# Kernel tuning notes

Measured on AMD Instinct MI355X. Metric: run time of the kernel, lower is better.

## Reference

```python
import jax, jax.numpy as jnp
import numpy as np
from jax import lax

DISP = 4   # max displacement for correlation -> 81 channels
KSZ = 3    # deform/gate conv kernel size


def conv2d(x, w, b=None):
    out = lax.conv_general_dilated(x, w, (1, 1), 'SAME',
                                   dimension_numbers=('NCHW', 'OIHW', 'NCHW'))
    if b is not None:
        out = out + b[None, :, None, None]
    return out


def correlation(x1, x2, d=DISP):
    # FlowNet-style cost volume, kernel_size=1: per-displacement channel-mean dot product.
    B, C, H, W = x1.shape
    x2p = jnp.pad(x2, ((0, 0), (0, 0), (d, d), (d, d)))
    outs = []
    for dy in range(2 * d + 1):
        for dx in range(2 * d + 1):
            shifted = lax.dynamic_slice(x2p, (0, 0, dy, dx), (B, C, H, W))
            outs.append(jnp.sum(x1 * shifted, axis=1) / C)
    return jnp.stack(outs, axis=1)  # [B, (2d+1)^2, H, W]


def bilinear_sample(img, y, x):
    # img: [B,C,H,W]; y,x: [B,H,W] float sample coords; zero padding outside.
    B, C, H, W = img.shape
    y0 = jnp.floor(y); x0 = jnp.floor(x)
    y1 = y0 + 1.0;     x1 = x0 + 1.0
    wy1 = y - y0; wx1 = x - x0
    wy0 = 1.0 - wy1; wx0 = 1.0 - wx1
    flat = img.reshape(B, C, H * W)

    def gather(yi, xi):
        valid = (yi >= 0) & (yi <= H - 1) & (xi >= 0) & (xi <= W - 1)
        yc = jnp.clip(yi, 0, H - 1).astype(jnp.int32)
        xc = jnp.clip(xi, 0, W - 1).astype(jnp.int32)
        idx = (yc * W + xc).reshape(B, 1, H * W)
        g = jnp.take_along_axis(flat, idx, axis=2).reshape(B, C, H, W)
        return g * valid.astype(img.dtype)[:, None]

    return (gather(y0, x0) * (wy0 * wx0)[:, None]
          + gather(y0, x1) * (wy0 * wx1)[:, None]
          + gather(y1, x0) * (wy1 * wx0)[:, None]
          + gather(y1, x1) * (wy1 * wx1)[:, None])


def deform_conv(img, offset, w, k=KSZ):
    # offset: [B, 2*k*k, H, W] with (dy, dx) pairs per kernel tap (row-major).
    B, C, H, W = img.shape
    pad = (k - 1) // 2
    ys = jnp.arange(H, dtype=img.dtype)[None, :, None]
    xs = jnp.arange(W, dtype=img.dtype)[None, None, :]
    out = jnp.zeros((B, w.shape[0], H, W), dtype=img.dtype)
    for kk in range(k * k):
        ky, kx = kk // k, kk % k
        y = ys + (ky - pad) + offset[:, 2 * kk]
        x = xs + (kx - pad) + offset[:, 2 * kk + 1]
        s = bilinear_sample(img, y, x)
        out = out + jnp.einsum('oc,bchw->bohw', w[:, :, ky, kx], s)
    return out


def linear_scale(x, std_multiplier=3.0):
    pos = x > 0
    cnt = jnp.sum(pos).astype(x.dtype)
    mean = jnp.sum(jnp.where(pos, x, 0.0)) / jnp.maximum(cnt, 1.0)
    var = jnp.sum(jnp.where(pos, (x - mean) ** 2, 0.0)) / jnp.maximum(cnt - 1.0, 1.0)
    ub = mean + std_multiplier * jnp.sqrt(var)
    ub = jnp.where(cnt >= 2.0, ub, 1.0)  # matches torch nan / empty-positive fallback
    return jnp.clip(x, 0.0, lax.stop_gradient(ub)) / ub


def setup_inputs() -> dict:
    key = jax.random.key(0)
    ks = jax.random.split(key, 10)
    B, C, H, W = 8, 256, 64, 64
    f = jnp.float32
    inp = {
        'inputs':   jax.random.normal(ks[0], (B, C, H, W), f),
        'in_state': jax.random.normal(ks[1], (B, C, H, W), f),
        'w_reset':  jax.random.normal(ks[2], (C, 2 * C, 3, 3), f) * 0.02,
        'b_reset':  jnp.zeros((C,), f),
        'w_update': jax.random.normal(ks[3], (C, 2 * C, 3, 3), f) * 0.02,
        'b_update': jnp.zeros((C,), f),
        'w_out':    jax.random.normal(ks[4], (C, 2 * C, 3, 3), f) * 0.02,
        'b_out':    jnp.zeros((C,), f),
        'w_offset': jax.random.normal(ks[5], (18, 81, 1, 1), f) * 0.01,
        'w_align':  jax.random.normal(ks[6], (C, C, 3, 3), f) * 0.01,
    }
    return inp


def reference(inputs, in_state, w_reset, b_reset, w_update, b_update,
              w_out, b_out, w_offset, w_align):
    # align_features: correlation -> 1x1 offset conv -> deformable conv
    corr = correlation(inputs, in_state)
    offset = conv2d(corr, w_offset)
    aligned = deform_conv(in_state, offset, w_align)
    # ConvGRU gates with linear-scaled relu gates
    stacked = jnp.concatenate([inputs, aligned], axis=1)
    update = linear_scale(jax.nn.relu(conv2d(stacked, w_update, b_update)))
    reset = linear_scale(jax.nn.relu(conv2d(stacked, w_reset, b_reset)))
    out_in = jax.nn.relu(conv2d(jnp.concatenate([inputs, in_state * reset], axis=1), w_out, b_out))
    new_state = in_state * (1.0 - update) + out_in * update
    return (new_state, new_state)  # (out_feat, new_state)
```

## Files before the change

kernel.cpp:

```cpp
#include <hip/hip_runtime.h>
#include <stdint.h>
#include <math.h>

typedef unsigned short u16;
typedef short bf16x8 __attribute__((ext_vector_type(8)));
typedef float f32x4 __attribute__((ext_vector_type(4)));

#define MFMA16x16x32(a,b,c) __builtin_amdgcn_mfma_f32_16x16x32_bf16((a),(b),(c),0,0,0)

typedef __attribute__((address_space(3))) void as3_void;
typedef const __attribute__((address_space(1))) void as1_void;

__device__ __forceinline__ void g2l16(const void* g, void* l){
#if __has_builtin(__builtin_amdgcn_global_load_lds)
  __builtin_amdgcn_global_load_lds((as1_void*)g, (as3_void*)l, 16, 0, 0);
#else
  *(int4*)l = *(const int4*)g;
#endif
}

__device__ __forceinline__ u16 f2bf(float f){
  uint32_t u = __builtin_bit_cast(uint32_t, f);
  u += 0x7fffu + ((u >> 16) & 1u);
  return (u16)(u >> 16);
}
__device__ __forceinline__ float bf2f(u16 h){
  uint32_t u = ((uint32_t)h) << 16;
  return __builtin_bit_cast(float, u);
}
__device__ __forceinline__ void unpack8(int4 v, float* o){
  uint32_t w0=(uint32_t)v.x, w1=(uint32_t)v.y, w2=(uint32_t)v.z, w3=(uint32_t)v.w;
  o[0]=__builtin_bit_cast(float, w0<<16); o[1]=__builtin_bit_cast(float, w0&0xffff0000u);
  o[2]=__builtin_bit_cast(float, w1<<16); o[3]=__builtin_bit_cast(float, w1&0xffff0000u);
  o[4]=__builtin_bit_cast(float, w2<<16); o[5]=__builtin_bit_cast(float, w2&0xffff0000u);
  o[6]=__builtin_bit_cast(float, w3<<16); o[7]=__builtin_bit_cast(float, w3&0xffff0000u);
}
__device__ __forceinline__ int iclampi(int v,int lo,int hi){ return v<lo?lo:(v>hi?hi:v); }

__global__ void k_repack(const float* __restrict__ w_reset, const float* __restrict__ b_reset,
                         const float* __restrict__ w_update, const float* __restrict__ b_update,
                         const float* __restrict__ w_out, const float* __restrict__ w_offset,
                         const float* __restrict__ w_align,
                         u16* __restrict__ wgate, u16* __restrict__ wout,
                         u16* __restrict__ walign, float* __restrict__ woff,
                         float* __restrict__ biascat){
  int idx = blockIdx.x * 256 + threadIdx.x;
  if (idx < 512*4608){
    int e = idx & 7, j = (idx >> 3) & 2047, chunk = idx >> 14;
    int nb = chunk & 1, kk = chunk >> 1;
    int l = j & 15, q = (j >> 4) & 3, t16 = (j >> 6) & 15, ks2 = j >> 10;
    int n = nb*256 + t16*16 + l;
    int tap = kk >> 3, ksin = kk & 7;
    int c = ksin*64 + ks2*32 + q*8 + e;
    int ky = tap/3, kx = tap%3;
    float v = (n < 256) ? w_update[((n*512 + c)*3 + ky)*3 + kx]
                        : w_reset[(((n-256)*512 + c)*3 + ky)*3 + kx];
    wgate[idx] = f2bf(v);
  }
  if (idx < 256*4608){
    int e = idx & 7, j = (idx >> 3) & 1023, chunk = idx >> 13;
    int nb = chunk & 1, kk = chunk >> 1;
    int l = j & 15, q = (j >> 4) & 3, t8 = (j >> 6) & 7, ks2 = j >> 9;
    int n = nb*128 + t8*16 + l;
    int tap = kk >> 3, ksin = kk & 7;
    int c = ksin*64 + ks2*32 + q*8 + e;
    int ky = tap/3, kx = tap%3;
    wout[idx] = f2bf(w_out[((n*512 + c)*3 + ky)*3 + kx]);
  }
  if (idx < 256*2304){
    int n = idx / 2304, k = idx % 2304;
    int tap = k >> 8, c = k & 255;
    int ky = tap/3, kx = tap%3;
    walign[idx] = f2bf(w_align[((n*256 + c)*3 + ky)*3 + kx]);
  }
  if (idx < 1458) woff[idx] = w_offset[idx] * (1.f/256.f);
  if (idx < 512) biascat[idx] = (idx < 256) ? b_update[idx] : b_reset[idx-256];
}

__global__ __launch_bounds__(256) void k_transform(const float* __restrict__ inputs,
    const float* __restrict__ in_state, u16* __restrict__ stacked,
    u16* __restrict__ stacked2, u16* __restrict__ x2pad){
  __shared__ u16 t1[64*264];
  __shared__ u16 t2[64*264];
  int tid = threadIdx.x, bh = blockIdx.x;
  int b = bh >> 6, h = bh & 63;
  int w = tid & 63, cq = tid >> 6;
  for (int i = 0; i < 64; ++i){
    int c = i*4 + cq;
    int gi = ((b*256 + c)*64 + h)*64 + w;
    t1[w*264 + c] = f2bf(inputs[gi]);
    t2[w*264 + c] = f2bf(in_state[gi]);
  }
  __syncthreads();
  int px = tid >> 2, cg = tid & 3;
#pragma unroll
  for (int u = 0; u < 8; ++u){
    int c = cg*64 + u*8;
    int4 v1 = *(const int4*)(t1 + px*264 + c);
    int4 v2 = *(const int4*)(t2 + px*264 + c);
    *(int4*)(stacked  + (((b*66 + h+1)*66) + (px+1))*512 + c) = v1;
    *(int4*)(stacked2 + (((b*66 + h+1)*66) + (px+1))*512 + c) = v1;
    *(int4*)(x2pad    + (((b*72 + h+4)*72) + (px+4))*256 + c) = v2;
  }
}

__global__ __launch_bounds__(256) void k_corr(const u16* __restrict__ stacked,
    const u16* __restrict__ x2pad, float* __restrict__ corr){
  __shared__ u16 lA[8192];
  __shared__ u16 lB[32768];
  int tid = threadIdx.x, idx = blockIdx.x;
  int b = idx >> 6, ty = (idx >> 3) & 7, tx = idx & 7;
  int h0 = ty*8, w0 = tx*8;
  int wave = tid >> 6, lane = tid & 63, l15 = lane & 15, quad = lane >> 4;
  f32x4 acc[4][4];
#pragma unroll
  for (int i=0;i<4;i++)
#pragma unroll
    for (int j=0;j<4;j++){ f32x4 z = {0.f,0.f,0.f,0.f}; acc[i][j] = z; }

  for (int s = 0; s < 2; ++s){
#pragma unroll
    for (int i = 0; i < 4; ++i){
      int j = tid + i*256;
      int ml = j & 15, q = (j>>4)&3, mt = (j>>6)&3, ks = j >> 8;
      int px = mt*16 + ml, py = px >> 3, pxx = px & 7;
      const u16* g = stacked + (((b*66 + h0+py+1)*66) + (w0+pxx+1))*512 + s*128 + ks*32 + q*8;
      g2l16(g, lA + j*8);
    }
#pragma unroll
    for (int i = 0; i < 16; ++i){
      int j = tid + i*256;
      int nl = j & 15, q = (j>>4)&3, nt = (j>>6)&15, ks = j >> 10;
      int qp = nt*16 + nl, qy = qp >> 4, qx = qp & 15;
      const u16* g = x2pad + (((b*72 + h0+qy)*72) + (w0+qx))*256 + s*128 + ks*32 + q*8;
      g2l16(g, lB + j*8);
    }
    __syncthreads();
#pragma unroll
    for (int ks = 0; ks < 4; ++ks){
      bf16x8 bv[4];
#pragma unroll
      for (int ni=0; ni<4; ++ni){
        int nt = wave*4 + ni;
        bv[ni] = *(const bf16x8*)(lB + (((ks*16 + nt)*4 + quad)*16 + l15)*8);
      }
#pragma unroll
      for (int mi=0; mi<4; ++mi){
        bf16x8 av = *(const bf16x8*)(lA + (((ks*4 + mi)*4 + quad)*16 + l15)*8);
#pragma unroll
        for (int ni=0; ni<4; ++ni) acc[mi][ni] = MFMA16x16x32(av, bv[ni], acc[mi][ni]);
      }
    }
    __syncthreads();
  }
#pragma unroll
  for (int mi=0; mi<4; ++mi){
#pragma unroll
    for (int ni=0; ni<4; ++ni){
      int n = wave*64 + ni*16 + l15;
      int qy = n >> 4, qx = n & 15;
#pragma unroll
      for (int r=0; r<4; ++r){
        int m = mi*16 + quad*4 + r;
        int py = m >> 3, pxx = m & 7;
        int dy = qy - py, dx = qx - pxx;
        if ((unsigned)dy <= 8u && (unsigned)dx <= 8u)
          corr[(((b*64 + h0+py)*64) + (w0+pxx))*81 + dy*9 + dx] = acc[mi][ni][r];
      }
    }
  }
}

__global__ __launch_bounds__(256) void k_offset(const float* __restrict__ corr,
    const float* __restrict__ woff, float* __restrict__ offs){
  __shared__ float lc[32*84];
  __shared__ float lw[18*84];
  int tid = threadIdx.x, blk = blockIdx.x;
  int row = blk >> 1, half = blk & 1;
  int base = row*5184 + half*32*81;
  for (int i = tid; i < 32*81; i += 256){
    int px = i / 81, d = i % 81;
    lc[px*84 + d] = corr[base + i];
  }
  for (int i = tid; i < 18*84; i += 256){
    int o = i / 84, d = i % 84;
    if (d < 81) lw[i] = woff[o*81 + d];
  }
  __syncthreads();
  int px = tid & 31, og = tid >> 5;
  for (int o = og; o < 18; o += 8){
    float s = 0.f;
#pragma unroll
    for (int dd = 0; dd < 20; ++dd){
      float4 a = *(const float4*)(lc + px*84 + dd*4);
      float4 wv = *(const float4*)(lw + o*84 + dd*4);
      s += a.x*wv.x + a.y*wv.y + a.z*wv.z + a.w*wv.w;
    }
    s += lc[px*84 + 80] * lw[o*84 + 80];
    offs[(row*64 + half*32 + px)*18 + o] = s;
  }
}

__global__ __launch_bounds__(256) void k_deform(const u16* __restrict__ x2pad,
    const float* __restrict__ offs, const u16* __restrict__ walign,
    u16* __restrict__ stacked){
  __shared__ u16 lA[16384];
  int tid = threadIdx.x, bh = blockIdx.x;
  int b = bh >> 6, h = bh & 63;
  int wave = tid >> 6, lane = tid & 63, l15 = lane & 15, quad = lane >> 4;
  int px = tid >> 2, cg = tid & 3;
  int mt_s = px >> 4, ml_s = px & 15;
  f32x4 acc[4][4];
#pragma unroll
  for (int i=0;i<4;i++)
#pragma unroll
    for (int j=0;j<4;j++){ f32x4 z = {0.f,0.f,0.f,0.f}; acc[i][j] = z; }

  for (int tap = 0; tap < 9; ++tap){
    int ky = tap/3, kx = tap%3;
    float offy = offs[(bh*64 + px)*18 + 2*tap];
    float offx = offs[(bh*64 + px)*18 + 2*tap + 1];
    float y = (float)(h + ky - 1) + offy;
    float x = (float)(px + kx - 1) + offx;
    float y0f = floorf(y), x0f = floorf(x);
    float wy1 = y - y0f, wx1 = x - x0f;
    float wy0 = 1.f - wy1, wx0 = 1.f - wx1;
    int iy0 = iclampi((int)y0f, -4, 67), ix0 = iclampi((int)x0f, -4, 67);
    int iy1 = iclampi((int)y0f + 1, -4, 67), ix1 = iclampi((int)x0f + 1, -4, 67);
    const u16* p00 = x2pad + (((b*72 + iy0+4)*72) + (ix0+4))*256 + cg*64;
    const u16* p01 = x2pad + (((b*72 + iy0+4)*72) + (ix1+4))*256 + cg*64;
    const u16* p10 = x2pad + (((b*72 + iy1+4)*72) + (ix0+4))*256 + cg*64;
    const u16* p11 = x2pad + (((b*72 + iy1+4)*72) + (ix1+4))*256 + cg*64;
    float w00 = wy0*wx0, w01 = wy0*wx1, w10 = wy1*wx0, w11 = wy1*wx1;
#pragma unroll
    for (int u = 0; u < 8; ++u){
      int4 v00 = *(const int4*)(p00 + u*8);
      int4 v01 = *(const int4*)(p01 + u*8);
      int4 v10 = *(const int4*)(p10 + u*8);
      int4 v11 = *(const int4*)(p11 + u*8);
      float a00[8], a01[8], a10[8], a11[8];
      unpack8(v00,a00); unpack8(v01,a01); unpack8(v10,a10); unpack8(v11,a11);
      union { u16 h2[8]; int4 v; } R;
#pragma unroll
      for (int jj = 0; jj < 8; ++jj)
        R.h2[jj] = f2bf(w00*a00[jj] + w01*a01[jj] + w10*a10[jj] + w11*a11[jj]);
      int ch = cg*64 + u*8;
      int ks = ch >> 5, q = (ch >> 3) & 3;
      *(int4*)(lA + (((ks*4 + mt_s)*4 + q)*16 + ml_s)*8) = R.v;
    }
    __syncthreads();
#pragma unroll
    for (int ks = 0; ks < 8; ++ks){
      bf16x8 bv[4];
#pragma unroll
      for (int ni=0; ni<4; ++ni){
        int n = wave*64 + ni*16 + l15;
        bv[ni] = *(const bf16x8*)(walign + n*2304 + tap*256 + ks*32 + quad*8);
      }
#pragma unroll
      for (int mi=0; mi<4; ++mi){
        bf16x8 av = *(const bf16x8*)(lA + (((ks*4 + mi)*4 + quad)*16 + l15)*8);
#pragma unroll
        for (int ni=0; ni<4; ++ni) acc[mi][ni] = MFMA16x16x32(av, bv[ni], acc[mi][ni]);
      }
    }
    __syncthreads();
  }
#pragma unroll
  for (int mi=0; mi<4; ++mi){
#pragma unroll
    for (int ni=0; ni<4; ++ni){
      int n = wave*64 + ni*16 + l15;
#pragma unroll
      for (int r=0; r<4; ++r){
        int m = mi*16 + quad*4 + r;
        stacked[(((b*66 + h+1)*66) + (m+1))*512 + 256 + n] = f2bf(acc[mi][ni][r]);
      }
    }
  }
}

__device__ __forceinline__ void stageA_half(u16* __restrict__ dst,
    const u16* __restrict__ in, int b, int h0, int kk, int hh, int tid){
  int tap = kk >> 3, ksin = kk & 7;
  int ky = tap/3, kx = tap - ky*3;
  const u16* abase = in + ((b*66 + h0 + ky)*66 + kx)*512 + ksin*64;
#pragma unroll
  for (int i = 0; i < 2; ++i){
    int pi = (tid >> 8)*2 + i;
    int ks2 = pi >> 1, blk = pi & 1;
    int j = (ks2<<10) | (blk<<9) | (hh<<8) | (tid & 255);
    int l = j & 15, q = (j >> 4) & 3;
    int t16 = ((j >> 6) & 3) | (hh<<2) | (blk<<3);
    int px = t16*16 + l, r = px >> 6, w = px & 63;
    g2l16(abase + (r*66 + w)*512 + ks2*32 + q*8, dst + j*8);
  }
}
__device__ __forceinline__ void stageB16_half(u16* __restrict__ dst,
    const u16* __restrict__ wts, int nb, int kk, int hh, int tid){
  const u16* wch = wts + (size_t)(kk*2 + nb) * 16384;
#pragma unroll
  for (int i = 0; i < 2; ++i){
    int j = (i<<10) | ((tid>>7)<<8) | (hh<<7) | (tid & 127);
    g2l16(wch + j*8, dst + j*8);
  }
}
__device__ __forceinline__ void stageB8(u16* __restrict__ dst,
    const u16* __restrict__ wts, int nb, int kk, int tid){
  const u16* wch = wts + (size_t)(kk*2 + nb) * 8192;
#pragma unroll
  for (int i = 0; i < 2; ++i){
    int j = (i<<9) | tid;
    g2l16(wch + j*8, dst + j*8);
  }
}

#define PHASE(QM, QN, WV, STG_STMT) do { \
  bf16x8 av_[4][2], bv_[2][2]; \
  _Pragma("unroll") \
  for (int m4=0;m4<4;++m4){ \
    _Pragma("unroll") \
    for (int k2=0;k2<2;++k2){ \
      int mrow = wm*8 + (QM)*4 + m4; \
      av_[m4][k2] = *(const bf16x8*)(Acur + (((k2*16 + mrow)*4 + quad)*16 + l15)*8); \
    } } \
  _Pragma("unroll") \
  for (int n2=0;n2<2;++n2){ \
    _Pragma("unroll") \
    for (int k2=0;k2<2;++k2){ \
      int ntl = wn*NI + (QN)*2 + n2; \
      bv_[n2][k2] = *(const bf16x8*)(Bcur + (((k2*NT + ntl)*4 + quad)*16 + l15)*8); \
    } } \
  STG_STMT; \
  asm volatile("" ::: "memory"); \
  __builtin_amdgcn_s_barrier(); \
  asm volatile("s_waitcnt lgkmcnt(0)" ::: "memory"); \
  __builtin_amdgcn_sched_barrier(0); \
  __builtin_amdgcn_s_setprio(1); \
  _Pragma("unroll") \
  for (int k2=0;k2<2;++k2){ \
    _Pragma("unroll") \
    for (int m4=0;m4<4;++m4){ \
      _Pragma("unroll") \
      for (int n2=0;n2<2;++n2){ \
        acc[(QM)*4+m4][(QN)*2+n2] = \
          MFMA16x16x32(av_[m4][k2], bv_[n2][k2], acc[(QM)*4+m4][(QN)*2+n2]); \
      } } } \
  __builtin_amdgcn_s_setprio(0); \
  __builtin_amdgcn_sched_barrier(0); \
  if (hasnext) { asm volatile("s_waitcnt vmcnt(" #WV ")" ::: "memory"); } \
  else         { asm volatile("s_waitcnt vmcnt(0)" ::: "memory"); } \
  asm volatile("" ::: "memory"); \
  __builtin_amdgcn_s_barrier(); \
} while(0)

template<int NT, bool STATS>
__global__ __launch_bounds__(512, 2) void k_conv256(const u16* __restrict__ in,
    const u16* __restrict__ wts, const float* __restrict__ bias,
    u16* __restrict__ outp, float* __restrict__ partials){
  constexpr int NI = NT / 4;
  __shared__ u16 lA[2][16384];
  __shared__ u16 lB[2][NT*1024];

  int tid = threadIdx.x, g = blockIdx.x;
  int work = (g & 7) * 32 + (g >> 3);
  int nb = work >> 7, mt = work & 127;
  int b = mt >> 4, h0 = (mt & 15) * 4;
  int wave = tid >> 6, lane = tid & 63, l15 = lane & 15, quad = lane >> 4;
  int wm = wave & 1, wn = wave >> 1;

  f32x4 acc[8][NI];
#pragma unroll
  for (int i=0;i<8;i++)
#pragma unroll
    for (int j=0;j<NI;j++){ f32x4 z = {0.f,0.f,0.f,0.f}; acc[i][j] = z; }

  if constexpr (NT == 16){
    stageA_half(&lA[0][0], in, b, h0, 0, 0, tid);
    stageB16_half(&lB[0][0], wts, nb, 0, 0, tid);
    stageA_half(&lA[0][0], in, b, h0, 0, 1, tid);
    stageB16_half(&lB[0][0], wts, nb, 0, 1, tid);
    asm volatile("s_waitcnt vmcnt(4)" ::: "memory");
  } else {
    stageA_half(&lA[0][0], in, b, h0, 0, 0, tid);
    stageB8(&lB[0][0], wts, nb, 0, tid);
    stageA_half(&lA[0][0], in, b, h0, 0, 1, tid);
    asm volatile("s_waitcnt vmcnt(2)" ::: "memory");
  }
  asm volatile("" ::: "memory");
  __builtin_amdgcn_s_barrier();

#pragma unroll 1
  for (int t = 0; t < 72; ++t){
    int d = t & 1;
    const u16* Acur = &lA[d][0];
    const u16* Bcur = &lB[d][0];
    u16* Anext = &lA[d^1][0];
    u16* Bnext = &lB[d^1][0];
    bool hasnext = (t < 71);
    int kn = t + 1;
    if constexpr (NT == 16){
      PHASE(0,0,2, if (hasnext) stageA_half(Anext, in, b, h0, kn, 0, tid));
      PHASE(0,1,6, if (hasnext) stageB16_half(Bnext, wts, nb, kn, 0, tid));
      PHASE(1,0,6, if (hasnext) stageA_half(Anext, in, b, h0, kn, 1, tid));
      PHASE(1,1,4, if (hasnext) stageB16_half(Bnext, wts, nb, kn, 1, tid));
    } else {
      PHASE(0,0,4, if (hasnext){ stageA_half(Anext, in, b, h0, kn, 0, tid);
                                 stageB8(Bnext, wts, nb, kn, tid); });
      PHASE(1,0,2, if (hasnext) stageA_half(Anext, in, b, h0, kn, 1, tid));
    }
  }

  float bvl[NI];
#pragma unroll
  for (int ni = 0; ni < NI; ++ni)
    bvl[ni] = bias[nb*(NT*16) + wn*(NI*16) + ni*16 + l15];
  float sc = 0.f, ss = 0.f, sq = 0.f;
#pragma unroll
  for (int mi=0; mi<8; ++mi){
#pragma unroll
    for (int ni=0; ni<NI; ++ni){
      int n = nb*(NT*16) + wn*(NI*16) + ni*16 + l15;
#pragma unroll
      for (int r=0; r<4; ++r){
        int m = wm*128 + mi*16 + quad*4 + r;
        int row = h0 + (m >> 6), w = m & 63;
        float v = acc[mi][ni][r] + bvl[ni];
        v = fmaxf(v, 0.f);
        outp[(((b*64 + row)*64) + w)*(NT*32) + n] = f2bf(v);
        if (STATS){ sc += (v > 0.f) ? 1.f : 0.f; ss += v; sq += v*v; }
      }
    }
  }
  if constexpr (STATS){
    __shared__ float red[8][3];
#pragma unroll
    for (int off = 32; off; off >>= 1){
      sc += __shfl_down(sc, off); ss += __shfl_down(ss, off); sq += __shfl_down(sq, off);
    }
    if (lane == 0){ red[wave][0]=sc; red[wave][1]=ss; red[wave][2]=sq; }
    __syncthreads();
    if (tid == 0){
      float a0=0,a1=0,a2=0;
      for (int w2=0; w2<8; ++w2){ a0+=red[w2][0]; a1+=red[w2][1]; a2+=red[w2][2]; }
      partials[work*3+0]=a0; partials[work*3+1]=a1; partials[work*3+2]=a2;
    }
  }
}

__global__ __launch_bounds__(256) void k_finalize(const float* __restrict__ partials,
                                                  float* __restrict__ ubs){
  __shared__ float red[4][6];
  int tid = threadIdx.x, lane = tid & 63, wave = tid >> 6;
  float cu=0,su=0,qu=0,cr=0,sr=0,qr=0;
  {
    float c = partials[tid*3+0], s = partials[tid*3+1], q = partials[tid*3+2];
    if (tid < 128){ cu=c; su=s; qu=q; } else { cr=c; sr=s; qr=q; }
  }
#pragma unroll
  for (int off = 32; off; off >>= 1){
    cu += __shfl_down(cu, off); su += __shfl_down(su, off); qu += __shfl_down(qu, off);
    cr += __shfl_down(cr, off); sr += __shfl_down(sr, off); qr += __shfl_down(qr, off);
  }
  if (lane == 0){ red[wave][0]=cu; red[wave][1]=su; red[wave][2]=qu;
                  red[wave][3]=cr; red[wave][4]=sr; red[wave][5]=qr; }
  __syncthreads();
  if (tid < 2){
    double C=0, S=0, Q=0;
    for (int w2=0; w2<4; ++w2){
      C += red[w2][tid*3+0]; S += red[w2][tid*3+1]; Q += red[w2][tid*3+2];
    }
    float ub = 1.f;
    if (C >= 2.0){
      double mean = S / C;
      double var = (Q - C*mean*mean) / (C - 1.0);
      if (var < 0.0) var = 0.0;
      ub = (float)(mean + 3.0*sqrt(var));
    }
    ubs[tid] = ub;
    ubs[2+tid] = 1.f/ub;
  }
}

__global__ __launch_bounds__(256) void k_mulreset(const u16* __restrict__ G,
    const u16* __restrict__ x2pad, const float* __restrict__ ubs,
    u16* __restrict__ stacked2){
  int tid = threadIdx.x, bh = blockIdx.x;
  int b = bh >> 6, h = bh & 63;
  int px = tid >> 2, cg = tid & 3;
  float ubr = ubs[1], inv = ubs[3];
#pragma unroll
  for (int u = 0; u < 8; ++u){
    int c = cg*64 + u*8;
    int4 gv = *(const int4*)(G + (bh*64 + px)*512 + 256 + c);
    int4 sv = *(const int4*)(x2pad + (((b*72 + h+4)*72) + (px+4))*256 + c);
    float gf[8], sf[8]; unpack8(gv, gf); unpack8(sv, sf);
    union { u16 h2[8]; int4 v; } R;
#pragma unroll
    for (int j=0;j<8;j++){
      float r = fminf(gf[j], ubr) * inv;
      R.h2[j] = f2bf(sf[j] * r);
    }
    *(int4*)(stacked2 + (((b*66 + h+1)*66) + (px+1))*512 + 256 + c) = R.v;
  }
}

__global__ __launch_bounds__(256) void k_final(const u16* __restrict__ G,
    const u16* __restrict__ O, const float* __restrict__ in_state,
    const float* __restrict__ ubs, float* __restrict__ dout){
  __shared__ float Q[64*65];
  __shared__ float P[64*65];
  int tid = threadIdx.x, bh = blockIdx.x;
  int b = bh >> 6, h = bh & 63;
  float ubu = ubs[0], inv = ubs[2];
  int px = tid >> 2, cs = (tid & 3)*16;
  int w = tid & 63, c4 = tid >> 6;
  for (int cb = 0; cb < 4; ++cb){
#pragma unroll
    for (int tt = 0; tt < 2; ++tt){
      int cl = cs + tt*8;
      int c = cb*64 + cl;
      int4 gv = *(const int4*)(G + (bh*64 + px)*512 + c);
      int4 ov = *(const int4*)(O + (bh*64 + px)*256 + c);
      float gf[8], of[8]; unpack8(gv, gf); unpack8(ov, of);
#pragma unroll
      for (int j=0;j<8;j++){
        float u = fminf(gf[j], ubu) * inv;
        Q[px*65 + cl + j] = u;
        P[px*65 + cl + j] = of[j]*u;
      }
    }
    __syncthreads();
    for (int i = 0; i < 16; ++i){
      int cl = i*4 + c4;
      int c = cb*64 + cl;
      int gidx = (((b*256 + c)*64) + h)*64 + w;
      float s = in_state[gidx];
      float v = s*(1.f - Q[w*65 + cl]) + P[w*65 + cl];
      dout[gidx] = v;
      dout[8388608 + gidx] = v;
    }
    __syncthreads();
  }
}

extern "C" void kernel_launch(void* const* d_in, const int* in_sizes, int n_in,
                              void* d_out, int out_size, void* d_ws, size_t ws_size,
                              hipStream_t stream){
  (void)in_sizes; (void)n_in; (void)out_size; (void)ws_size;
  const float* inputs   = (const float*)d_in[0];
  const float* in_state = (const float*)d_in[1];
  const float* w_reset  = (const float*)d_in[2];
  const float* b_reset  = (const float*)d_in[3];
  const float* w_update = (const float*)d_in[4];
  const float* b_update = (const float*)d_in[5];
  const float* w_out    = (const float*)d_in[6];
  const float* b_out    = (const float*)d_in[7];
  const float* w_offset = (const float*)d_in[8];
  const float* w_align  = (const float*)d_in[9];
  float* dout = (float*)d_out;

  char* ws = (char*)d_ws;
  size_t off = 0;
  auto alloc = [&](size_t bytes)->char*{
    char* p = ws + off; off = (off + bytes + 255) & ~(size_t)255; return p;
  };
  const size_t x2pad_b   = 8ull*72*72*256*2;
  const size_t stacked_b = 8ull*66*66*512*2;
  u16* x2pad    = (u16*)alloc(x2pad_b);
  u16* stacked  = (u16*)alloc(stacked_b);
  u16* stacked2 = (u16*)alloc(stacked_b);
  float* corr   = (float*)alloc(8ull*64*64*81*4);
  float* offs   = (float*)alloc(8ull*64*64*18*4);
  u16* G        = (u16*)alloc(8ull*64*64*512*2);
  u16* O        = (u16*)alloc(8ull*64*64*256*2);
  u16* wgate    = (u16*)alloc(512ull*4608*2);
  u16* woutb    = (u16*)alloc(256ull*4608*2);
  u16* walignb  = (u16*)alloc(256ull*2304*2);
  float* woff   = (float*)alloc(1458*4);
  float* biascat= (float*)alloc(512*4);
  float* partials=(float*)alloc(1024*3*4);
  float* ubs    = (float*)alloc(4*4);

  hipMemsetAsync(x2pad,    0, x2pad_b,   stream);
  hipMemsetAsync(stacked,  0, stacked_b, stream);
  hipMemsetAsync(stacked2, 0, stacked_b, stream);

  k_repack<<<9216, 256, 0, stream>>>(w_reset, b_reset, w_update, b_update, w_out,
                                     w_offset, w_align, wgate, woutb, walignb, woff, biascat);
  k_transform<<<512, 256, 0, stream>>>(inputs, in_state, stacked, stacked2, x2pad);
  k_corr<<<512, 256, 0, stream>>>(stacked, x2pad, corr);
  k_offset<<<1024, 256, 0, stream>>>(corr, woff, offs);
  k_deform<<<512, 256, 0, stream>>>(x2pad, offs, walignb, stacked);
  k_conv256<16, true><<<256, 512, 0, stream>>>(stacked, wgate, biascat, G, partials);
  k_finalize<<<1, 256, 0, stream>>>(partials, ubs);
  k_mulreset<<<512, 256, 0, stream>>>(G, x2pad, ubs, stacked2);
  k_conv256<8, false><<<256, 512, 0, stream>>>(stacked2, woutb, b_out, O, nullptr);
  k_final<<<512, 256, 0, stream>>>(G, O, in_state, ubs, dout);
}
```

Baseline: 701.9 us.

## Split conv K-step phases by k-half instead of M/N quadrants

Restructures the double-buffered conv GEMM so that each phase consumes one 32-wide k-half of the staged tile rather than an M/N quadrant. Staging of A and B is reorganised per k-half, B fragments are reused across two phases in the NT=16 variant, and some vmcnt waits are dropped or changed. The aim is fewer redundant LDS fragment reads and a finer overlap of global-to-LDS loads with MFMA work. It also changes barrier and wait timing, which risks hazards if a k-half is consumed before its staging load has landed.

```diff
diff --git a/kernel.cpp b/kernel.cpp
--- a/kernel.cpp
+++ b/kernel.cpp
@@ -280,57 +280,45 @@
   }
 }
 
-__device__ __forceinline__ void stageA_half(u16* __restrict__ dst,
-    const u16* __restrict__ in, int b, int h0, int kk, int hh, int tid){
+__device__ __forceinline__ void stageA_k(u16* __restrict__ dst,
+    const u16* __restrict__ in, int b, int h0, int kk, int ks2, int tid){
   int tap = kk >> 3, ksin = kk & 7;
   int ky = tap/3, kx = tap - ky*3;
-  const u16* abase = in + ((b*66 + h0 + ky)*66 + kx)*512 + ksin*64;
+  const u16* abase = in + ((b*66 + h0 + ky)*66 + kx)*512 + ksin*64 + ks2*32;
 #pragma unroll
   for (int i = 0; i < 2; ++i){
-    int pi = (tid >> 8)*2 + i;
-    int ks2 = pi >> 1, blk = pi & 1;
-    int j = (ks2<<10) | (blk<<9) | (hh<<8) | (tid & 255);
-    int l = j & 15, q = (j >> 4) & 3;
-    int t16 = ((j >> 6) & 3) | (hh<<2) | (blk<<3);
+    int j = (ks2<<10) | (i<<9) | tid;
+    int l = j & 15, q = (j >> 4) & 3, t16 = (j >> 6) & 15;
     int px = t16*16 + l, r = px >> 6, w = px & 63;
-    g2l16(abase + (r*66 + w)*512 + ks2*32 + q*8, dst + j*8);
-  }
-}
-__device__ __forceinline__ void stageB16_half(u16* __restrict__ dst,
-    const u16* __restrict__ wts, int nb, int kk, int hh, int tid){
+    g2l16(abase + (r*66 + w)*512 + q*8, dst + j*8);
+  }
+}
+__device__ __forceinline__ void stageB16_k(u16* __restrict__ dst,
+    const u16* __restrict__ wts, int nb, int kk, int ks2, int tid){
   const u16* wch = wts + (size_t)(kk*2 + nb) * 16384;
 #pragma unroll
   for (int i = 0; i < 2; ++i){
-    int j = (i<<10) | ((tid>>7)<<8) | (hh<<7) | (tid & 127);
+    int j = (ks2<<10) | (i<<9) | tid;
     g2l16(wch + j*8, dst + j*8);
   }
 }
-__device__ __forceinline__ void stageB8(u16* __restrict__ dst,
-    const u16* __restrict__ wts, int nb, int kk, int tid){
+__device__ __forceinline__ void stageB8_k(u16* __restrict__ dst,
+    const u16* __restrict__ wts, int nb, int kk, int ks2, int tid){
   const u16* wch = wts + (size_t)(kk*2 + nb) * 8192;
-#pragma unroll
-  for (int i = 0; i < 2; ++i){
-    int j = (i<<9) | tid;
-    g2l16(wch + j*8, dst + j*8);
-  }
-}
-
-#define PHASE(QM, QN, WV, STG_STMT) do { \
-  bf16x8 av_[4][2], bv_[2][2]; \
+  int j = (ks2<<9) | tid;
+  g2l16(wch + j*8, dst + j*8);
+}
+
+#define PHASE16(MH, K2, LOADB, STG_STMT, WV) do { \
+  bf16x8 av_[4]; \
   _Pragma("unroll") \
-  for (int m4=0;m4<4;++m4){ \
+  for (int m4=0;m4<4;++m4) \
+    av_[m4] = *(const bf16x8*)(Acur + ((((K2)*16 + wm*8 + (MH)*4 + m4)*4 + quad)*16 + l15)*8); \
+  if constexpr (LOADB){ \
     _Pragma("unroll") \
-    for (int k2=0;k2<2;++k2){ \
-      int mrow = wm*8 + (QM)*4 + m4; \
-      av_[m4][k2] = *(const bf16x8*)(Acur + (((k2*16 + mrow)*4 + quad)*16 + l15)*8); \
-    } } \
-  _Pragma("unroll") \
-  for (int n2=0;n2<2;++n2){ \
-    _Pragma("unroll") \
-    for (int k2=0;k2<2;++k2){ \
-      int ntl = wn*NI + (QN)*2 + n2; \
-      bv_[n2][k2] = *(const bf16x8*)(Bcur + (((k2*NT + ntl)*4 + quad)*16 + l15)*8); \
-    } } \
+    for (int ni=0;ni<4;++ni) \
+      bv_[ni] = *(const bf16x8*)(Bcur + ((((K2)*16 + wn*4 + ni)*4 + quad)*16 + l15)*8); \
+  } \
   STG_STMT; \
   asm volatile("" ::: "memory"); \
   __builtin_amdgcn_s_barrier(); \
@@ -338,17 +326,44 @@
   __builtin_amdgcn_sched_barrier(0); \
   __builtin_amdgcn_s_setprio(1); \
   _Pragma("unroll") \
-  for (int k2=0;k2<2;++k2){ \
+  for (int m4=0;m4<4;++m4){ \
     _Pragma("unroll") \
-    for (int m4=0;m4<4;++m4){ \
-      _Pragma("unroll") \
-      for (int n2=0;n2<2;++n2){ \
-        acc[(QM)*4+m4][(QN)*2+n2] = \
-          MFMA16x16x32(av_[m4][k2], bv_[n2][k2], acc[(QM)*4+m4][(QN)*2+n2]); \
-      } } } \
+    for (int ni=0;ni<4;++ni) \
+      acc[(MH)*4+m4][ni] = MFMA16x16x32(av_[m4], bv_[ni], acc[(MH)*4+m4][ni]); \
+  } \
   __builtin_amdgcn_s_setprio(0); \
   __builtin_amdgcn_sched_barrier(0); \
-  if (hasnext) { asm volatile("s_waitcnt vmcnt(" #WV ")" ::: "memory"); } \
+  if ((WV) >= 0){ \
+    if (hasnext) { asm volatile("s_waitcnt vmcnt(%0)" :: "i"((WV) < 0 ? 0 : (WV)) : "memory"); } \
+    else         { asm volatile("s_waitcnt vmcnt(0)" ::: "memory"); } \
+  } \
+  asm volatile("" ::: "memory"); \
+  __builtin_amdgcn_s_barrier(); \
+} while(0)
+
+#define PHASE8(K2, STG_STMT, WV) do { \
+  bf16x8 av_[8]; \
+  _Pragma("unroll") \
+  for (int m8=0;m8<8;++m8) \
+    av_[m8] = *(const bf16x8*)(Acur + ((((K2)*16 + wm*8 + m8)*4 + quad)*16 + l15)*8); \
+  _Pragma("unroll") \
+  for (int ni=0;ni<2;++ni) \
+    bv_[ni] = *(const bf16x8*)(Bcur + ((((K2)*8 + wn*2 + ni)*4 + quad)*16 + l15)*8); \
+  STG_STMT; \
+  asm volatile("" ::: "memory"); \
+  __builtin_amdgcn_s_barrier(); \
+  asm volatile("s_waitcnt lgkmcnt(0)" ::: "memory"); \
+  __builtin_amdgcn_sched_barrier(0); \
+  __builtin_amdgcn_s_setprio(1); \
+  _Pragma("unroll") \
+  for (int m8=0;m8<8;++m8){ \
+    _Pragma("unroll") \
+    for (int ni=0;ni<2;++ni) \
+      acc[m8][ni] = MFMA16x16x32(av_[m8], bv_[ni], acc[m8][ni]); \
+  } \
+  __builtin_amdgcn_s_setprio(0); \
+  __builtin_amdgcn_sched_barrier(0); \
+  if (hasnext) { asm volatile("s_waitcnt vmcnt(%0)" :: "i"(WV) : "memory"); } \
   else         { asm volatile("s_waitcnt vmcnt(0)" ::: "memory"); } \
   asm volatile("" ::: "memory"); \
   __builtin_amdgcn_s_barrier(); \
@@ -376,16 +391,17 @@
     for (int j=0;j<NI;j++){ f32x4 z = {0.f,0.f,0.f,0.f}; acc[i][j] = z; }
 
   if constexpr (NT == 16){
-    stageA_half(&lA[0][0], in, b, h0, 0, 0, tid);
-    stageB16_half(&lB[0][0], wts, nb, 0, 0, tid);
-    stageA_half(&lA[0][0], in, b, h0, 0, 1, tid);
-    stageB16_half(&lB[0][0], wts, nb, 0, 1, tid);
+    stageA_k(&lA[0][0], in, b, h0, 0, 0, tid);
+    stageB16_k(&lB[0][0], wts, nb, 0, 0, tid);
+    stageA_k(&lA[0][0], in, b, h0, 0, 1, tid);
+    stageB16_k(&lB[0][0], wts, nb, 0, 1, tid);
     asm volatile("s_waitcnt vmcnt(4)" ::: "memory");
   } else {
-    stageA_half(&lA[0][0], in, b, h0, 0, 0, tid);
-    stageB8(&lB[0][0], wts, nb, 0, tid);
-    stageA_half(&lA[0][0], in, b, h0, 0, 1, tid);
-    asm volatile("s_waitcnt vmcnt(2)" ::: "memory");
+    stageA_k(&lA[0][0], in, b, h0, 0, 0, tid);
+    stageB8_k(&lB[0][0], wts, nb, 0, 0, tid);
+    stageA_k(&lA[0][0], in, b, h0, 0, 1, tid);
+    stageB8_k(&lB[0][0], wts, nb, 0, 1, tid);
+    asm volatile("s_waitcnt vmcnt(3)" ::: "memory");
   }
   asm volatile("" ::: "memory");
   __builtin_amdgcn_s_barrier();
@@ -400,14 +416,17 @@
     bool hasnext = (t < 71);
     int kn = t + 1;
     if constexpr (NT == 16){
-      PHASE(0,0,2, if (hasnext) stageA_half(Anext, in, b, h0, kn, 0, tid));
-      PHASE(0,1,6, if (hasnext) stageB16_half(Bnext, wts, nb, kn, 0, tid));
-      PHASE(1,0,6, if (hasnext) stageA_half(Anext, in, b, h0, kn, 1, tid));
-      PHASE(1,1,4, if (hasnext) stageB16_half(Bnext, wts, nb, kn, 1, tid));
+      bf16x8 bv_[4];
+      PHASE16(0, 0, 1, if (hasnext) stageA_k(Anext, in, b, h0, kn, 0, tid), -1);
+      PHASE16(1, 0, 0, if (hasnext) stageB16_k(Bnext, wts, nb, kn, 0, tid), 4);
+      PHASE16(0, 1, 1, if (hasnext) stageA_k(Anext, in, b, h0, kn, 1, tid), -1);
+      PHASE16(1, 1, 0, if (hasnext) stageB16_k(Bnext, wts, nb, kn, 1, tid), 4);
     } else {
-      PHASE(0,0,4, if (hasnext){ stageA_half(Anext, in, b, h0, kn, 0, tid);
-                                 stageB8(Bnext, wts, nb, kn, tid); });
-      PHASE(1,0,2, if (hasnext) stageA_half(Anext, in, b, h0, kn, 1, tid));
+      bf16x8 bv_[2];
+      PHASE8(0, if (hasnext){ stageA_k(Anext, in, b, h0, kn, 0, tid);
+                              stageB8_k(Bnext, wts, nb, kn, 0, tid); }, 3);
+      PHASE8(1, if (hasnext){ stageA_k(Anext, in, b, h0, kn, 1, tid);
+                              stageB8_k(Bnext, wts, nb, kn, 1, tid); }, 3);
     }
   }
 
```

Measured after the change: 669.4 us. -4.6%, faster.
